# Optimization experiments

Hardware: AMD Instinct MI355X
Metric: run time of the kernel (lower is better)

## Reference

```python
import jax, jax.numpy as jnp
import numpy as np

B, K, D = 512, 20, 256


def _build_adjs(K):
    def tri(N):
        a = np.zeros((N, N), np.int32)
        a[0, 1] = a[1, 0] = 1
        a[0, 2] = a[2, 0] = 1
        a[1, 2] = a[2, 1] = 1
        return a
    adj1 = tri(3)
    adj2 = tri(3 + 3 * K)
    adj3 = tri(3 + 6 * K)
    for i in range(K):
        for c in range(3):
            adj2[c, 3 + c * K + i] = adj2[3 + c * K + i, c] = 2
            adj3[c, 3 + c * K + i] = adj3[3 + c * K + i, c] = 2
            adj3[c, 3 + 3 * K + c * K + i] = adj3[3 + 3 * K + c * K + i, c] = 3
    return jnp.asarray(adj1), jnp.asarray(adj2), jnp.asarray(adj3)

ADJ1, ADJ2, ADJ3 = _build_adjs(K)


def _rgat(h, adj, W, a_src, a_dst):
    # h: [B,N,F]; adj: [N,N] int relation labels (0 = no edge);
    # W: [R,F,E] per-relation projection; a_src/a_dst: [R,E] attention vecs.
    R = W.shape[0]
    Wh = jnp.einsum('bnf,rfe->brne', h, W)                      # [B,R,N,E]
    e = jax.nn.leaky_relu(
        jnp.einsum('brne,re->brn', Wh, a_src)[..., :, None]
        + jnp.einsum('brne,re->brn', Wh, a_dst)[..., None, :],
        negative_slope=0.2)                                     # [B,R,N,N]
    rel = jnp.arange(1, R + 1, dtype=jnp.int32)
    mask = (adj[None, :, :] == rel[:, None, None])[None]        # [1,R,N,N]
    alpha = jnp.where(mask, jax.nn.softmax(jnp.where(mask, e, -1e9), axis=-1), 0.0)
    return jax.nn.elu(jnp.einsum('brnm,brme->bne', alpha, Wh))  # [B,N,E]


def setup_inputs():
    key = jax.random.key(0)
    ks = jax.random.split(key, 40)
    n = lambda i, shp: jax.random.normal(ks[i], shp, dtype=jnp.float32)
    w = lambda i, shp: 0.02 * jax.random.normal(ks[i], shp, dtype=jnp.float32)
    inp = {
        'scene_tv': n(0, (B, 1, 1024)), 'face_tv': n(1, (B, 1, 1024)), 'text_tv': n(2, (B, 1, 2048)),
        'scene_refs': n(3, (B, K, 1024)), 'face_refs': n(4, (B, K, 1024)), 'text_refs': n(5, (B, K, 2048)),
        'scene_ra': n(6, (B, K, 1024)), 'face_ra': n(7, (B, K, 1024)), 'text_ra': n(8, (B, K, 1024)),
        'Ws1': w(9, (1024, D)), 'bs1': jnp.zeros((D,), jnp.float32),
        'Wf1': w(10, (1024, D)), 'bf1': jnp.zeros((D,), jnp.float32),
        'Wt1': w(11, (2048, D)), 'bt1': jnp.zeros((D,), jnp.float32),
        'G1W': w(12, (1, D, D)), 'G1as': w(13, (1, D)), 'G1ad': w(14, (1, D)),
        'Ws2': w(15, (1024, D)), 'bs2': jnp.zeros((D,), jnp.float32),
        'Wf2': w(16, (1024, D)), 'bf2': jnp.zeros((D,), jnp.float32),
        'Wt2': w(17, (2048, D)), 'bt2': jnp.zeros((D,), jnp.float32),
        'G2W': w(18, (2, D, D)), 'G2as': w(19, (2, D)), 'G2ad': w(20, (2, D)),
        'Ws3': w(21, (1024, D)), 'bs3': jnp.zeros((D,), jnp.float32),
        'Wf3': w(22, (1024, D)), 'bf3': jnp.zeros((D,), jnp.float32),
        'Wt3': w(23, (1024, D)), 'bt3': jnp.zeros((D,), jnp.float32),
        'G3W': w(24, (3, D, D)), 'G3as': w(25, (3, D)), 'G3ad': w(26, (3, D)),
    }
    return inp


def reference(scene_tv, face_tv, text_tv, scene_refs, face_refs, text_refs,
              scene_ra, face_ra, text_ra,
              Ws1, bs1, Wf1, bf1, Wt1, bt1, G1W, G1as, G1ad,
              Ws2, bs2, Wf2, bf2, Wt2, bt2, G2W, G2as, G2ad,
              Ws3, bs3, Wf3, bf3, Wt3, bt3, G3W, G3as, G3ad):
    # Stage 1: Basic_Emotion_Graph (3 nodes, 1 relation type)
    nodes1 = jnp.concatenate([scene_tv @ Ws1 + bs1,
                              face_tv @ Wf1 + bf1,
                              text_tv @ Wt1 + bt1], axis=1)      # [B,3,D]
    g1 = _rgat(nodes1, ADJ1, G1W, G1as, G1ad)
    # Stage 2: Indirect_Emotion_Extended_Graph (3+3K nodes, 2 relation types)
    nodes2 = jnp.concatenate([g1,
                              scene_refs @ Ws2 + bs2,
                              face_refs @ Wf2 + bf2,
                              text_refs @ Wt2 + bt2], axis=1)    # [B,3+3K,D]
    g2 = _rgat(nodes2, ADJ2, G2W, G2as, G2ad)
    # Stage 3: Direct_Emotion_Extended_Graph (3+6K nodes, 3 relation types)
    nodes3 = jnp.concatenate([g2,
                              scene_ra @ Ws3 + bs3,
                              face_ra @ Wf3 + bf3,
                              text_ra @ Wt3 + bt3], axis=1)      # [B,3+6K,D]
    return _rgat(nodes3, ADJ3, G3W, G3as, G3ad)
```

## Files before the change

kernel.cpp:

```cpp
#include <hip/hip_runtime.h>
#include <hip/hip_bf16.h>
#include <math.h>

typedef __bf16 bf16_t;
typedef __bf16 bf16x8 __attribute__((ext_vector_type(8)));
typedef __bf16 bf16x4 __attribute__((ext_vector_type(4)));
typedef float  floatx4 __attribute__((ext_vector_type(4)));

#define NB 512
#define DI 256

__device__ __forceinline__ float lrelu_f(float x){ return x >= 0.f ? x : 0.2f*x; }
__device__ __forceinline__ float elu_f(float x){ return x > 0.f ? x : expm1f(x); }

__global__ __launch_bounds__(256)
void detect_k(const void* __restrict__ probe, int* __restrict__ flag)
{
    __shared__ int cnt_s;
    if (threadIdx.x == 0) cnt_s = 0;
    __syncthreads();
    const unsigned short* u = (const unsigned short*)probe;
    int c = 0;
    for (int i = threadIdx.x; i < 16384; i += 256) {
        int e = (u[i] >> 7) & 0xFF;
        if (e >= 0x90) c++;
    }
    atomicAdd(&cnt_s, c);
    __syncthreads();
    if (threadIdx.x == 0) *flag = (cnt_s > 64) ? 1 : 0;
}

struct SCEnt { const void* s; bf16_t* d; int n; };
struct SCArgs { SCEnt e[16]; int cnt; };

__global__ __launch_bounds__(256)
void smallconv_k(SCArgs a, const int* __restrict__ flag)
{
    int isf = *flag;
    for (int k = 0; k < a.cnt; ++k) {
        int n = a.e[k].n;
        for (int i = threadIdx.x + blockIdx.x * 256; i < n; i += gridDim.x * 256) {
            float v = isf ? ((const float*)a.e[k].s)[i]
                          : (float)((const bf16_t*)a.e[k].s)[i];
            a.e[k].d[i] = (bf16_t)v;
        }
    }
}

struct TDesc { const void* W; size_t eoff; bf16_t* WT; int K; int tstart; };
struct TArgs { TDesc d[15]; int nd; };

__global__ __launch_bounds__(256)
void transpose_multi_k(TArgs ta, const int* __restrict__ flagp)
{
    __shared__ bf16_t tile[32][33];
    const int isf = *flagp;
    const int bx = blockIdx.x;
    int di = 0;
    while (di + 1 < ta.nd && bx >= ta.d[di + 1].tstart) ++di;
    const void* Wbase = ta.d[di].W;
    const size_t eoff = ta.d[di].eoff;
    bf16_t* WT        = ta.d[di].WT;
    const int K       = ta.d[di].K;
    const int ti      = bx - ta.d[di].tstart;
    const int tk      = K >> 5;
    const int kb      = (ti % tk) * 32;
    const int nb      = (ti / tk) * 32;
    const int tx = threadIdx.x & 31, ty = threadIdx.x >> 5;
    #pragma unroll
    for (int rr = 0; rr < 4; ++rr) {
        int r = ty + rr * 8;
        size_t idx = eoff + (size_t)(kb + r) * 256 + nb + tx;
        tile[r][tx] = isf ? (bf16_t)((const float*)Wbase)[idx]
                          : ((const bf16_t*)Wbase)[idx];
    }
    __syncthreads();
    #pragma unroll
    for (int rr = 0; rr < 4; ++rr) {
        int r = ty + rr * 8;
        WT[(size_t)(nb + r) * K + kb + tx] = tile[tx][r];
    }
}

#define BM 64
#define BN 64
#define BK 32
#define LST 40

struct GDesc {
    const void* A; const bf16_t* WT; const bf16_t* bias; bf16_t* out;
    int Kin, in_stride_b, in_off, rows_pb, a_is_ext, out_stride_b, out_off, mb_start;
};
struct GArgs { GDesc d[9]; int nd; };

__global__ __launch_bounds__(256)
void gemm_multi_k(GArgs ga, const int* __restrict__ flagp)
{
    __shared__ bf16_t As[BM * LST];
    __shared__ bf16_t Bs[BN * LST];

    const int mb = blockIdx.x >> 2;
    const int n0 = (blockIdx.x & 3) * BN;
    int di = 0;
    while (di + 1 < ga.nd && mb >= ga.d[di + 1].mb_start) ++di;

    const void*   A        = ga.d[di].A;
    const bf16_t* WT       = ga.d[di].WT;
    const bf16_t* bias     = ga.d[di].bias;
    bf16_t*       out      = ga.d[di].out;
    const int Kin          = ga.d[di].Kin;
    const int in_stride_b  = ga.d[di].in_stride_b;
    const int in_off       = ga.d[di].in_off;
    const int rows_pb      = ga.d[di].rows_pb;
    const int out_stride_b = ga.d[di].out_stride_b;
    const int out_off      = ga.d[di].out_off;
    const int a_fp32 = ga.d[di].a_is_ext ? *flagp : 0;

    const int t  = threadIdx.x;
    const int m0 = (mb - ga.d[di].mb_start) * BM;

    const int s_row = t >> 2;
    const int s_col = (t & 3) * 8;

    const int g_row = m0 + s_row;
    const int b_idx = g_row / rows_pb;
    const int i_idx = g_row - b_idx * rows_pb;
    const size_t a_base = (size_t)(b_idx * in_stride_b + in_off + i_idx) * Kin + s_col;
    const bf16_t* w_ptr = WT + (size_t)(n0 + s_row) * Kin + s_col;

    const int wave = t >> 6;
    const int lane = t & 63;
    const int wr = (wave >> 1) * 32;
    const int wc = (wave & 1) * 32;
    const int lm = lane & 15;
    const int lk = (lane >> 4) * 8;

    floatx4 acc[2][2] = {};

    for (int kk = 0; kk < Kin; kk += BK) {
        bf16x8 av;
        if (a_fp32) {
            const float* ap = (const float*)A + a_base + kk;
            float4 f0 = *(const float4*)ap;
            float4 f1 = *(const float4*)(ap + 4);
            av[0] = (bf16_t)f0.x; av[1] = (bf16_t)f0.y;
            av[2] = (bf16_t)f0.z; av[3] = (bf16_t)f0.w;
            av[4] = (bf16_t)f1.x; av[5] = (bf16_t)f1.y;
            av[6] = (bf16_t)f1.z; av[7] = (bf16_t)f1.w;
        } else {
            av = *(const bf16x8*)((const bf16_t*)A + a_base + kk);
        }
        bf16x8 wv = *(const bf16x8*)(w_ptr + kk);
        *(bf16x8*)(&As[s_row * LST + s_col]) = av;
        *(bf16x8*)(&Bs[s_row * LST + s_col]) = wv;
        __syncthreads();

        bf16x8 af0 = *(const bf16x8*)(&As[(wr      + lm) * LST + lk]);
        bf16x8 af1 = *(const bf16x8*)(&As[(wr + 16 + lm) * LST + lk]);
        bf16x8 bf0 = *(const bf16x8*)(&Bs[(wc      + lm) * LST + lk]);
        bf16x8 bf1 = *(const bf16x8*)(&Bs[(wc + 16 + lm) * LST + lk]);

        acc[0][0] = __builtin_amdgcn_mfma_f32_16x16x32_bf16(af0, bf0, acc[0][0], 0, 0, 0);
        acc[0][1] = __builtin_amdgcn_mfma_f32_16x16x32_bf16(af0, bf1, acc[0][1], 0, 0, 0);
        acc[1][0] = __builtin_amdgcn_mfma_f32_16x16x32_bf16(af1, bf0, acc[1][0], 0, 0, 0);
        acc[1][1] = __builtin_amdgcn_mfma_f32_16x16x32_bf16(af1, bf1, acc[1][1], 0, 0, 0);
        __syncthreads();
    }

    const int q = lane >> 4;
    #pragma unroll
    for (int i = 0; i < 2; ++i)
      #pragma unroll
      for (int j = 0; j < 2; ++j)
        #pragma unroll
        for (int r = 0; r < 4; ++r) {
            int row = m0 + wr + i * 16 + q * 4 + r;
            int col = n0 + wc + j * 16 + lm;
            int bb = row / rows_pb;
            int ii = row - bb * rows_pb;
            float v = acc[i][j][r];
            if (bias) v += (float)bias[col];
            out[(size_t)(bb * out_stride_b + out_off + ii) * DI + col] = (bf16_t)v;
        }
}

struct SDesc { const bf16_t* Wh; const bf16_t* as_; const bf16_t* ad_;
               float* s; float* d; int bstart; };
struct SArgs { SDesc e[3]; int nd; };

__global__ __launch_bounds__(256)
void scores_multi_k(SArgs sa)
{
    const int bx = blockIdx.x;
    int di = 0;
    while (di + 1 < sa.nd && bx >= sa.e[di + 1].bstart) ++di;
    const bf16_t* Wh    = sa.e[di].Wh;
    const bf16_t* a_src = sa.e[di].as_;
    const bf16_t* a_dst = sa.e[di].ad_;
    float* src = sa.e[di].s;
    float* dst = sa.e[di].d;

    int wid  = (bx - sa.e[di].bstart) * 4 + (threadIdx.x >> 6);
    int lane = threadIdx.x & 63;
    bf16x4 wv = *(const bf16x4*)(Wh + (size_t)wid * DI + lane * 4);
    bf16x4 sv = *(const bf16x4*)(a_src + lane * 4);
    bf16x4 dv = *(const bf16x4*)(a_dst + lane * 4);
    float s = 0.f, d = 0.f;
    #pragma unroll
    for (int i = 0; i < 4; ++i) {
        float w = (float)wv[i];
        s += w * (float)sv[i];
        d += w * (float)dv[i];
    }
    #pragma unroll
    for (int off = 32; off > 0; off >>= 1) {
        s += __shfl_down(s, off);
        d += __shfl_down(d, off);
    }
    if (lane == 0) { src[wid] = s; dst[wid] = d; }
}

__device__ __forceinline__ float hub20(const bf16_t* __restrict__ Wh,
                                       const float* __restrict__ s,
                                       const float* __restrict__ d,
                                       int b, int c, int e)
{
    int base = b * 63 + 3 + c * 20;
    float ss = s[b * 63 + c];
    float ev[20], mx = -1e30f;
    #pragma unroll
    for (int i = 0; i < 20; ++i) { ev[i] = lrelu_f(ss + d[base + i]); mx = fmaxf(mx, ev[i]); }
    float sw = 0.f, acc = 0.f;
    #pragma unroll
    for (int i = 0; i < 20; ++i) {
        float w = expf(ev[i] - mx);
        sw  += w;
        acc += w * (float)Wh[(size_t)(base + i) * DI + e];
    }
    return acc / sw;
}

__device__ __forceinline__ float hub_tri(const bf16_t* __restrict__ Wh1,
                                         const float* __restrict__ s1,
                                         const float* __restrict__ d1,
                                         int b, int c, int e)
{
    int m0 = (c == 0) ? 1 : 0, m1 = (c == 2) ? 1 : 2;
    float ss = s1[b * 3 + c];
    float e0 = lrelu_f(ss + d1[b * 3 + m0]);
    float e1 = lrelu_f(ss + d1[b * 3 + m1]);
    float mx = fmaxf(e0, e1);
    float w0 = expf(e0 - mx), w1 = expf(e1 - mx);
    return (w0 * (float)Wh1[(size_t)(b * 3 + m0) * DI + e] +
            w1 * (float)Wh1[(size_t)(b * 3 + m1) * DI + e]) / (w0 + w1);
}

__global__ __launch_bounds__(256)
void agg1_k(const bf16_t* __restrict__ Wh1, const float* __restrict__ s1,
            const float* __restrict__ d1, bf16_t* __restrict__ nodes2)
{
    int blk = blockIdx.x;
    int b = blk / 3, n = blk - b * 3;
    int e = threadIdx.x;
    float v = hub_tri(Wh1, s1, d1, b, n, e);
    nodes2[(size_t)(b * 63 + n) * DI + e] = (bf16_t)elu_f(v);
}

__global__ __launch_bounds__(256)
void agg2_k(const bf16_t* __restrict__ Wh1, const bf16_t* __restrict__ Wh2,
            const float* __restrict__ s1, const float* __restrict__ d1,
            const float* __restrict__ s2, const float* __restrict__ d2,
            bf16_t* __restrict__ nodes3)
{
    int blk = blockIdx.x;
    int b = blk / 63, n = blk - b * 63;
    int e = threadIdx.x;
    float v;
    if (n >= 3) {
        int c = (n - 3) / 20;
        v = (float)Wh2[(size_t)(b * 63 + c) * DI + e];
    } else {
        v = hub_tri(Wh1, s1, d1, b, n, e) + hub20(Wh2, s2, d2, b, n, e);
    }
    nodes3[(size_t)(b * 123 + n) * DI + e] = (bf16_t)elu_f(v);
}

__global__ __launch_bounds__(256)
void agg3_k(const bf16_t* __restrict__ Wh1, const bf16_t* __restrict__ Wh2,
            const bf16_t* __restrict__ Wh3,
            const float* __restrict__ s1, const float* __restrict__ d1,
            const float* __restrict__ s2, const float* __restrict__ d2,
            const float* __restrict__ s3, const float* __restrict__ d3,
            void* __restrict__ out, const int* __restrict__ flagp)
{
    int isf = *flagp;
    int blk = blockIdx.x;
    int b = blk / 123, n = blk - b * 123;
    int e = threadIdx.x;
    float v;
    if (n >= 63) {
        int c = (n - 63) / 20;
        v = (float)Wh3[(size_t)(b * 63 + c) * DI + e];
    } else if (n >= 3) {
        int c = (n - 3) / 20;
        v = (float)Wh2[(size_t)(b * 63 + c) * DI + e];
    } else {
        v = hub_tri(Wh1, s1, d1, b, n, e)
          + hub20(Wh2, s2, d2, b, n, e)
          + hub20(Wh3, s3, d3, b, n, e);
    }
    float r = elu_f(v);
    size_t oi = (size_t)(b * 123 + n) * DI + e;
    if (isf) ((float*)out)[oi] = r;
    else     ((bf16_t*)out)[oi] = (bf16_t)r;
}

extern "C" void kernel_launch(void* const* d_in, const int* in_sizes, int n_in,
                              void* d_out, int out_size, void* d_ws, size_t ws_size,
                              hipStream_t stream)
{
    (void)in_sizes; (void)n_in; (void)out_size; (void)ws_size;
    const void *scene_tv=d_in[0], *face_tv=d_in[1], *text_tv=d_in[2],
               *scene_refs=d_in[3], *face_refs=d_in[4], *text_refs=d_in[5],
               *scene_ra=d_in[6], *face_ra=d_in[7], *text_ra=d_in[8],
               *Ws1=d_in[9],  *bs1=d_in[10], *Wf1=d_in[11], *bf1=d_in[12],
               *Wt1=d_in[13], *bt1=d_in[14],
               *G1W=d_in[15], *G1as=d_in[16], *G1ad=d_in[17],
               *Ws2=d_in[18], *bs2=d_in[19], *Wf2=d_in[20], *bf2=d_in[21],
               *Wt2=d_in[22], *bt2=d_in[23],
               *G2W=d_in[24], *G2as=d_in[25], *G2ad=d_in[26],
               *Ws3=d_in[27], *bs3=d_in[28], *Wf3=d_in[29], *bf3=d_in[30],
               *Wt3=d_in[31], *bt3=d_in[32],
               *G3W=d_in[33], *G3as=d_in[34], *G3ad=d_in[35];

    char* p = (char*)d_ws;
    auto carveB = [&](size_t elems) -> bf16_t* { bf16_t* r = (bf16_t*)p; p += ((elems*2 + 255) & ~(size_t)255); return r; };
    auto carveF = [&](size_t elems) -> float*  { float*  r = (float*)p;  p += ((elems*4 + 255) & ~(size_t)255); return r; };
    auto carveI = [&]() -> int* { int* r = (int*)p; p += 256; return r; };

    int* flag = carveI();

    bf16_t* Ws1T = carveB(1024*256); bf16_t* Wf1T = carveB(1024*256); bf16_t* Wt1T = carveB(2048*256);
    bf16_t* Ws2T = carveB(1024*256); bf16_t* Wf2T = carveB(1024*256); bf16_t* Wt2T = carveB(2048*256);
    bf16_t* Ws3T = carveB(1024*256); bf16_t* Wf3T = carveB(1024*256); bf16_t* Wt3T = carveB(1024*256);
    bf16_t* G1WT = carveB(256*256);
    bf16_t* G2WT = carveB(2*256*256);
    bf16_t* G3WT = carveB(3*256*256);

    bf16_t* cb[9];
    for (int i = 0; i < 9; ++i) cb[i] = carveB(256);
    bf16_t* a1s = carveB(256); bf16_t* a1d = carveB(256);
    bf16_t* a2s = carveB(512); bf16_t* a2d = carveB(512);
    bf16_t* a3s = carveB(768); bf16_t* a3d = carveB(768);

    bf16_t* nodes1 = carveB((size_t)NB*3*DI);
    bf16_t* nodes2 = carveB((size_t)NB*63*DI);
    bf16_t* nodes3 = carveB((size_t)NB*123*DI);
    bf16_t* Wh1    = carveB((size_t)NB*3*DI);
    bf16_t* Wh2    = carveB((size_t)NB*63*DI);
    bf16_t* Wh3    = carveB((size_t)NB*63*DI);
    float* s1s = carveF(NB*3);  float* s1d = carveF(NB*3);
    float* s2s = carveF(NB*63); float* s2d = carveF(NB*63);
    float* s3s = carveF(NB*63); float* s3d = carveF(NB*63);

    detect_k<<<1, 256, 0, stream>>>(Ws1, flag);

    SCArgs sca;
    const void* ssrc[15] = { bs1, bf1, bt1, bs2, bf2, bt2, bs3, bf3, bt3,
                             G1as, G1ad, G2as, G2ad, G3as, G3ad };
    bf16_t* sdst[15] = { cb[0],cb[1],cb[2],cb[3],cb[4],cb[5],cb[6],cb[7],cb[8],
                         a1s, a1d, a2s, a2d, a3s, a3d };
    int sn[15] = { 256,256,256,256,256,256,256,256,256, 256,256,512,512,768,768 };
    for (int i = 0; i < 15; ++i) { sca.e[i].s = ssrc[i]; sca.e[i].d = sdst[i]; sca.e[i].n = sn[i]; }
    sca.cnt = 15;
    smallconv_k<<<1, 256, 0, stream>>>(sca, flag);

    TArgs ta; ta.nd = 0; int tcum = 0;
    auto addT = [&](const void* W, size_t eoff, bf16_t* WT, int K) {
        ta.d[ta.nd].W = W; ta.d[ta.nd].eoff = eoff; ta.d[ta.nd].WT = WT;
        ta.d[ta.nd].K = K; ta.d[ta.nd].tstart = tcum;
        tcum += (K / 32) * 8; ta.nd++;
    };
    addT(Ws1, 0, Ws1T, 1024); addT(Wf1, 0, Wf1T, 1024); addT(Wt1, 0, Wt1T, 2048);
    addT(Ws2, 0, Ws2T, 1024); addT(Wf2, 0, Wf2T, 1024); addT(Wt2, 0, Wt2T, 2048);
    addT(Ws3, 0, Ws3T, 1024); addT(Wf3, 0, Wf3T, 1024); addT(Wt3, 0, Wt3T, 1024);
    addT(G1W, 0,      G1WT,          256);
    addT(G2W, 0,      G2WT,          256); addT(G2W, 65536,  G2WT + 65536,  256);
    addT(G3W, 0,      G3WT,          256); addT(G3W, 65536,  G3WT + 65536,  256);
    addT(G3W, 131072, G3WT + 131072, 256);
    transpose_multi_k<<<tcum, 256, 0, stream>>>(ta, flag);

    auto addG = [](GArgs& A, int& cum, const void* Ain, int Kin, int isb, int ioff,
                   int rpb, int ext, const bf16_t* WT, const bf16_t* bias,
                   bf16_t* out, int osb, int ooff, int M) {
        GDesc& g = A.d[A.nd];
        g.A = Ain; g.WT = WT; g.bias = bias; g.out = out;
        g.Kin = Kin; g.in_stride_b = isb; g.in_off = ioff; g.rows_pb = rpb;
        g.a_is_ext = ext; g.out_stride_b = osb; g.out_off = ooff; g.mb_start = cum;
        cum += M / 64; A.nd++;
    };

    GArgs pg; pg.nd = 0; int pc = 0;
    addG(pg, pc, scene_tv,   1024,  1, 0,  1, 1, Ws1T, cb[0], nodes1,   3,   0, NB);
    addG(pg, pc, face_tv,    1024,  1, 0,  1, 1, Wf1T, cb[1], nodes1,   3,   1, NB);
    addG(pg, pc, text_tv,    2048,  1, 0,  1, 1, Wt1T, cb[2], nodes1,   3,   2, NB);
    addG(pg, pc, scene_refs, 1024, 20, 0, 20, 1, Ws2T, cb[3], nodes2,  63,   3, NB*20);
    addG(pg, pc, face_refs,  1024, 20, 0, 20, 1, Wf2T, cb[4], nodes2,  63,  23, NB*20);
    addG(pg, pc, text_refs,  2048, 20, 0, 20, 1, Wt2T, cb[5], nodes2,  63,  43, NB*20);
    addG(pg, pc, scene_ra,   1024, 20, 0, 20, 1, Ws3T, cb[6], nodes3, 123,  63, NB*20);
    addG(pg, pc, face_ra,    1024, 20, 0, 20, 1, Wf3T, cb[7], nodes3, 123,  83, NB*20);
    addG(pg, pc, text_ra,    1024, 20, 0, 20, 1, Wt3T, cb[8], nodes3, 123, 103, NB*20);
    gemm_multi_k<<<pc * 4, 256, 0, stream>>>(pg, flag);

    GArgs g1; g1.nd = 0; int c1 = 0;
    addG(g1, c1, nodes1, 256, 3, 0, 3, 0, G1WT, nullptr, Wh1, 3, 0, NB*3);
    gemm_multi_k<<<c1 * 4, 256, 0, stream>>>(g1, flag);

    SArgs s1a; s1a.nd = 1;
    s1a.e[0].Wh = Wh1; s1a.e[0].as_ = a1s; s1a.e[0].ad_ = a1d;
    s1a.e[0].s = s1s; s1a.e[0].d = s1d; s1a.e[0].bstart = 0;
    scores_multi_k<<<NB*3/4, 256, 0, stream>>>(s1a);
    agg1_k<<<NB*3, 256, 0, stream>>>(Wh1, s1s, s1d, nodes2);

    GArgs g2; g2.nd = 0; int c2 = 0;
    addG(g2, c2, nodes2, 256, 63, 0,  3, 0, G2WT,         nullptr, Wh1,  3, 0, NB*3);
    addG(g2, c2, nodes2, 256, 63, 0, 63, 0, G2WT + 65536, nullptr, Wh2, 63, 0, NB*63);
    gemm_multi_k<<<c2 * 4, 256, 0, stream>>>(g2, flag);

    SArgs s2a; s2a.nd = 2;
    s2a.e[0].Wh = Wh1; s2a.e[0].as_ = a2s;       s2a.e[0].ad_ = a2d;
    s2a.e[0].s = s1s;  s2a.e[0].d = s1d;         s2a.e[0].bstart = 0;
    s2a.e[1].Wh = Wh2; s2a.e[1].as_ = a2s + 256; s2a.e[1].ad_ = a2d + 256;
    s2a.e[1].s = s2s;  s2a.e[1].d = s2d;         s2a.e[1].bstart = NB*3/4;
    scores_multi_k<<<NB*3/4 + NB*63/4, 256, 0, stream>>>(s2a);
    agg2_k<<<NB*63, 256, 0, stream>>>(Wh1, Wh2, s1s, s1d, s2s, s2d, nodes3);

    GArgs g3; g3.nd = 0; int c3 = 0;
    addG(g3, c3, nodes3, 256, 123,  0,  3, 0, G3WT,          nullptr, Wh1,  3, 0, NB*3);
    addG(g3, c3, nodes3, 256, 123,  0, 63, 0, G3WT + 65536,  nullptr, Wh2, 63, 0, NB*63);
    addG(g3, c3, nodes3, 256, 123,  0,  3, 0, G3WT + 131072, nullptr, Wh3, 63, 0, NB*3);
    addG(g3, c3, nodes3, 256, 123, 63, 60, 0, G3WT + 131072, nullptr, Wh3, 63, 3, NB*60);
    gemm_multi_k<<<c3 * 4, 256, 0, stream>>>(g3, flag);

    SArgs s3a; s3a.nd = 3;
    s3a.e[0].Wh = Wh1; s3a.e[0].as_ = a3s;       s3a.e[0].ad_ = a3d;
    s3a.e[0].s = s1s;  s3a.e[0].d = s1d;         s3a.e[0].bstart = 0;
    s3a.e[1].Wh = Wh2; s3a.e[1].as_ = a3s + 256; s3a.e[1].ad_ = a3d + 256;
    s3a.e[1].s = s2s;  s3a.e[1].d = s2d;         s3a.e[1].bstart = NB*3/4;
    s3a.e[2].Wh = Wh3; s3a.e[2].as_ = a3s + 512; s3a.e[2].ad_ = a3d + 512;
    s3a.e[2].s = s3s;  s3a.e[2].d = s3d;         s3a.e[2].bstart = NB*3/4 + NB*63/4;
    scores_multi_k<<<NB*3/4 + 2*(NB*63/4), 256, 0, stream>>>(s3a);
    agg3_k<<<NB*123, 256, 0, stream>>>(Wh1, Wh2, Wh3, s1s, s1d, s2s, s2d, s3s, s3d,
                                       d_out, flag);
}
```

Baseline: 646.4 us.

## Prefetch next K-tile into registers and remap blocks across XCDs in multi-GEMM

The GEMM main loop now issues the global loads for the next K-slice into registers right after the shared-memory barrier, so those loads overlap the MFMA work on the current slice. Block indices are also remapped so that consecutive M-blocks land on different XCDs while the four N-tiles of an M-block share one XCD, aiming for better L2 reuse of the A rows. The remap assumes the grid size is a multiple of 32. It also depends on the number of M-blocks being a multiple of 8, otherwise some blocks could go out of range, and the register prefetch adds some register pressure.

```diff
diff --git a/kernel.cpp b/kernel.cpp
--- a/kernel.cpp
+++ b/kernel.cpp
@@ -99,8 +99,12 @@
     __shared__ bf16_t As[BM * LST];
     __shared__ bf16_t Bs[BN * LST];
 
-    const int mb = blockIdx.x >> 2;
-    const int n0 = (blockIdx.x & 3) * BN;
+    const int bx  = blockIdx.x;
+    const int xcd = bx & 7;
+    const int w   = bx >> 3;
+    const int mb  = (w >> 2) * 8 + xcd;
+    const int n0  = (w & 3) * BN;
+
     int di = 0;
     while (di + 1 < ga.nd && mb >= ga.d[di + 1].mb_start) ++di;
 
@@ -137,23 +141,41 @@
 
     floatx4 acc[2][2] = {};
 
+    float4 f0, f1;
+    bf16x8 avr, wvr;
+    if (a_fp32) {
+        const float* ap = (const float*)A + a_base;
+        f0 = *(const float4*)ap;
+        f1 = *(const float4*)(ap + 4);
+    } else {
+        avr = *(const bf16x8*)((const bf16_t*)A + a_base);
+    }
+    wvr = *(const bf16x8*)(w_ptr);
+
     for (int kk = 0; kk < Kin; kk += BK) {
         bf16x8 av;
         if (a_fp32) {
-            const float* ap = (const float*)A + a_base + kk;
-            float4 f0 = *(const float4*)ap;
-            float4 f1 = *(const float4*)(ap + 4);
             av[0] = (bf16_t)f0.x; av[1] = (bf16_t)f0.y;
             av[2] = (bf16_t)f0.z; av[3] = (bf16_t)f0.w;
             av[4] = (bf16_t)f1.x; av[5] = (bf16_t)f1.y;
             av[6] = (bf16_t)f1.z; av[7] = (bf16_t)f1.w;
         } else {
-            av = *(const bf16x8*)((const bf16_t*)A + a_base + kk);
+            av = avr;
         }
-        bf16x8 wv = *(const bf16x8*)(w_ptr + kk);
         *(bf16x8*)(&As[s_row * LST + s_col]) = av;
-        *(bf16x8*)(&Bs[s_row * LST + s_col]) = wv;
+        *(bf16x8*)(&Bs[s_row * LST + s_col]) = wvr;
         __syncthreads();
+
+        if (kk + BK < Kin) {
+            if (a_fp32) {
+                const float* ap = (const float*)A + a_base + kk + BK;
+                f0 = *(const float4*)ap;
+                f1 = *(const float4*)(ap + 4);
+            } else {
+                avr = *(const bf16x8*)((const bf16_t*)A + a_base + kk + BK);
+            }
+            wvr = *(const bf16x8*)(w_ptr + kk + BK);
+        }
 
         bf16x8 af0 = *(const bf16x8*)(&As[(wr      + lm) * LST + lk]);
         bf16x8 af1 = *(const bf16x8*)(&As[(wr + 16 + lm) * LST + lk]);
```

Measured after the change: 603.2 us. 6.7% less time.
